# Kernel tuning notes

Measured on AMD Instinct MI355X. Metric: run time of the kernel, lower is better.

## Reference

```python
import jax, jax.numpy as jnp
import numpy as np

GRID = 7
COORD = 5.0
NO_OBJ = 0.5


def _corners(xywh, r, c):
    # xywh: [...,4] with (x_cell, y_cell, w, h); r,c broadcastable grid indices
    x, y, w, h = xywh[..., 0], xywh[..., 1], xywh[..., 2], xywh[..., 3]
    cx = (x + c) / GRID
    cy = (y + r) / GRID
    return cx - w / 2, cy - h / 2, cx + w / 2, cy + h / 2


def _iou(a, b):
    ax1, ay1, ax2, ay2 = a
    bx1, by1, bx2, by2 = b
    iw = jnp.maximum(jnp.minimum(ax2, bx2) - jnp.maximum(ax1, bx1), 0.0)
    ih = jnp.maximum(jnp.minimum(ay2, by2) - jnp.maximum(ay1, by1), 0.0)
    inter = iw * ih
    area_a = (ax2 - ax1) * (ay2 - ay1)
    area_b = (bx2 - bx1) * (by2 - by1)
    union = area_a + area_b - inter
    return jnp.where(union > 0, inter / jnp.where(union > 0, union, 1.0), 0.0)


def setup_inputs() -> dict:
    key = jax.random.key(0)
    k1, k2, k3 = jax.random.split(key, 3)
    B = 8192
    data = jax.random.uniform(k1, (B, GRID, GRID, 30), dtype=jnp.float32)
    labels = jax.random.uniform(k2, (B, GRID, GRID, 30), dtype=jnp.float32)
    # obj flag at channel 4 must be exactly 1 for obj cells
    obj = jax.random.randint(k3, (B, GRID, GRID), 0, 2).astype(jnp.float32)
    labels = labels.at[..., 4].set(obj)
    return {"data": data, "labels": labels}


def reference(data, labels):
    B = data.shape[0]
    r = jnp.arange(GRID, dtype=data.dtype)[None, :, None]  # row index -> y offset
    c = jnp.arange(GRID, dtype=data.dtype)[None, None, :]  # col index -> x offset

    box1 = _corners(data[..., 0:4], r, c)
    box2 = _corners(data[..., 5:9], r, c)
    gt = _corners(labels[..., 0:4], r, c)

    iou1 = _iou(box1, gt)  # [B,7,7]
    iou2 = _iou(box2, gt)
    resp1 = iou1 >= iou2

    xy1 = jnp.sum((data[..., 0:2] - labels[..., 0:2]) ** 2, -1)
    xy2 = jnp.sum((data[..., 5:7] - labels[..., 5:7]) ** 2, -1)
    wh1 = jnp.sum((jnp.sqrt(data[..., 2:4]) - jnp.sqrt(labels[..., 2:4])) ** 2, -1)
    wh2 = jnp.sum((jnp.sqrt(data[..., 7:9]) - jnp.sqrt(labels[..., 7:9])) ** 2, -1)

    d4, d9 = data[..., 4], data[..., 9]
    co = COORD * jnp.where(resp1, xy1, xy2)
    wh = COORD * jnp.where(resp1, wh1, wh2)
    confi = jnp.where(resp1, (d4 - iou1) ** 2, (d9 - iou2) ** 2)
    noobj_in = NO_OBJ * jnp.where(resp1, d9 ** 2, d4 ** 2)
    cls = jnp.sum((data[..., 10:] - labels[..., 10:]) ** 2, -1)

    m = (labels[..., 4] == 1).astype(data.dtype)
    obj_loss = m * (co + wh + confi + noobj_in + cls)
    noobj_loss = (1.0 - m) * NO_OBJ * (d4 ** 2 + d9 ** 2)
    return jnp.sum(obj_loss + noobj_loss) / B
```

## Files before the change

kernel.cpp:

```cpp
#include <hip/hip_runtime.h>

#define COORD 5.0f
#define NO_OBJ 0.5f
#define NCELLS (8192 * 49)
#define INV_B (1.0f / 8192.0f)

#define CPB 128
#define FPT (CPB * 30)
#define NTILES (NCELLS / CPB)
#define NPBLK 512

__device__ __forceinline__ float iou_calc(float ax1, float ay1, float ax2, float ay2,
                                          float bx1, float by1, float bx2, float by2) {
    float iw = fminf(ax2, bx2) - fmaxf(ax1, bx1);
    iw = fmaxf(iw, 0.0f);
    float ih = fminf(ay2, by2) - fmaxf(ay1, by1);
    ih = fmaxf(ih, 0.0f);
    float inter = iw * ih;
    float area_a = (ax2 - ax1) * (ay2 - ay1);
    float area_b = (bx2 - bx1) * (by2 - by1);
    float uni = area_a + area_b - inter;
    return uni > 0.0f ? inter / uni : 0.0f;
}

__device__ __forceinline__ void stage_tile(const float* __restrict__ g, float* s, int tid) {
#pragma unroll
    for (int j = 0; j < 7; j++) {
        __builtin_amdgcn_global_load_lds(
            (const __attribute__((address_space(1))) void*)(g + j * 512 + tid * 4),
            (__attribute__((address_space(3))) void*)(s + j * 512 + tid * 4), 16, 0, 0);
    }
#pragma unroll
    for (int j = 0; j < 2; j++) {
        __builtin_amdgcn_global_load_lds(
            (const __attribute__((address_space(1))) void*)(g + 3584 + j * 128 + tid),
            (__attribute__((address_space(3))) void*)(s + 3584 + j * 128 + tid), 4, 0, 0);
    }
}

__device__ __forceinline__ float cell_loss(const float* __restrict__ sd,
                                           const float* __restrict__ sl,
                                           int idx, int tid) {
    const int cell = idx % 49;
    const float r = (float)(cell / 7);
    const float c = (float)(cell % 7);

    float d[30], l[30];
    const float2* dp = (const float2*)(sd + tid * 30);
    const float2* lp = (const float2*)(sl + tid * 30);
#pragma unroll
    for (int i = 0; i < 15; i++) {
        float2 v = dp[i];
        d[2 * i] = v.x; d[2 * i + 1] = v.y;
        float2 w2 = lp[i];
        l[2 * i] = w2.x; l[2 * i + 1] = w2.y;
    }

    const float inv_g = 1.0f / 7.0f;
    float cx1 = (d[0] + c) * inv_g, cy1 = (d[1] + r) * inv_g;
    float b1x1 = cx1 - d[2] * 0.5f, b1y1 = cy1 - d[3] * 0.5f;
    float b1x2 = cx1 + d[2] * 0.5f, b1y2 = cy1 + d[3] * 0.5f;
    float cx2 = (d[5] + c) * inv_g, cy2 = (d[6] + r) * inv_g;
    float b2x1 = cx2 - d[7] * 0.5f, b2y1 = cy2 - d[8] * 0.5f;
    float b2x2 = cx2 + d[7] * 0.5f, b2y2 = cy2 + d[8] * 0.5f;
    float gx = (l[0] + c) * inv_g, gy = (l[1] + r) * inv_g;
    float gx1 = gx - l[2] * 0.5f, gy1 = gy - l[3] * 0.5f;
    float gx2 = gx + l[2] * 0.5f, gy2 = gy + l[3] * 0.5f;

    float iou1 = iou_calc(b1x1, b1y1, b1x2, b1y2, gx1, gy1, gx2, gy2);
    float iou2 = iou_calc(b2x1, b2y1, b2x2, b2y2, gx1, gy1, gx2, gy2);
    bool resp1 = iou1 >= iou2;

    float xy1 = (d[0] - l[0]) * (d[0] - l[0]) + (d[1] - l[1]) * (d[1] - l[1]);
    float xy2 = (d[5] - l[5]) * (d[5] - l[5]) + (d[6] - l[6]) * (d[6] - l[6]);
    float s2 = sqrtf(d[2]) - sqrtf(l[2]);
    float s3 = sqrtf(d[3]) - sqrtf(l[3]);
    float wh1 = s2 * s2 + s3 * s3;
    float s7 = sqrtf(d[7]) - sqrtf(l[7]);
    float s8 = sqrtf(d[8]) - sqrtf(l[8]);
    float wh2 = s7 * s7 + s8 * s8;

    float d4 = d[4], d9 = d[9];
    float co = COORD * (resp1 ? xy1 : xy2);
    float wh = COORD * (resp1 ? wh1 : wh2);
    float ci = resp1 ? (d4 - iou1) * (d4 - iou1) : (d9 - iou2) * (d9 - iou2);
    float noobj_in = NO_OBJ * (resp1 ? d9 * d9 : d4 * d4);
    float cls = 0.0f;
#pragma unroll
    for (int i = 10; i < 30; i++) {
        float t = d[i] - l[i];
        cls += t * t;
    }

    return (l[4] == 1.0f) ? (co + wh + ci + noobj_in + cls)
                          : NO_OBJ * (d4 * d4 + d9 * d9);
}

__global__ __launch_bounds__(CPB) void yolo_loss_kernel(
    const float* __restrict__ data, const float* __restrict__ labels,
    float* __restrict__ ws) {
    __shared__ float sd[2][FPT];
    __shared__ float sl[2][FPT];

    const int tid = threadIdx.x;
    float acc = 0.0f;
    int cur = 0;

    stage_tile(data + (size_t)blockIdx.x * FPT, sd[0], tid);
    stage_tile(labels + (size_t)blockIdx.x * FPT, sl[0], tid);

    for (int i = blockIdx.x; i < NTILES; i += NPBLK) {
        __syncthreads();
        const int nxt = i + NPBLK;
        if (nxt < NTILES) {
            stage_tile(data + (size_t)nxt * FPT, sd[cur ^ 1], tid);
            stage_tile(labels + (size_t)nxt * FPT, sl[cur ^ 1], tid);
        }
        acc += cell_loss(sd[cur], sl[cur], i * CPB + tid, tid);
        cur ^= 1;
    }
    acc *= INV_B;

#pragma unroll
    for (int off = 32; off > 0; off >>= 1)
        acc += __shfl_down(acc, off, 64);

    __syncthreads();
    if ((tid & 63) == 0) sd[0][tid >> 6] = acc;
    __syncthreads();
    if (tid == 0) ws[blockIdx.x] = sd[0][0] + sd[0][1];
}

__global__ __launch_bounds__(256) void reduce_kernel(const float* __restrict__ ws,
                                                     float* __restrict__ out) {
    float s = 0.0f;
    for (int i = threadIdx.x; i < NPBLK; i += 256) s += ws[i];
#pragma unroll
    for (int off = 32; off > 0; off >>= 1)
        s += __shfl_down(s, off, 64);
    __shared__ float w[4];
    if ((threadIdx.x & 63) == 0) w[threadIdx.x >> 6] = s;
    __syncthreads();
    if (threadIdx.x == 0) out[0] = w[0] + w[1] + w[2] + w[3];
}

extern "C" void kernel_launch(void* const* d_in, const int* in_sizes, int n_in,
                              void* d_out, int out_size, void* d_ws, size_t ws_size,
                              hipStream_t stream) {
    const float* data = (const float*)d_in[0];
    const float* labels = (const float*)d_in[1];
    float* out = (float*)d_out;
    float* ws = (float*)d_ws;

    yolo_loss_kernel<<<NPBLK, CPB, 0, stream>>>(data, labels, ws);
    reduce_kernel<<<1, 256, 0, stream>>>(ws, out);
}
```

Before: 114.4 us.

## Use single-wave blocks with barrier-free two-ahead async prefetch via vmcnt waits

```diff
diff --git a/kernel.cpp b/kernel.cpp
--- a/kernel.cpp
+++ b/kernel.cpp
@@ -5,10 +5,10 @@
 #define NCELLS (8192 * 49)
 #define INV_B (1.0f / 8192.0f)
 
-#define CPB 128
+#define CPB 64
 #define FPT (CPB * 30)
 #define NTILES (NCELLS / CPB)
-#define NPBLK 512
+#define NPBLK 1280
 
 __device__ __forceinline__ float iou_calc(float ax1, float ay1, float ax2, float ay2,
                                           float bx1, float by1, float bx2, float by2) {
@@ -27,14 +27,14 @@
 #pragma unroll
     for (int j = 0; j < 7; j++) {
         __builtin_amdgcn_global_load_lds(
-            (const __attribute__((address_space(1))) void*)(g + j * 512 + tid * 4),
-            (__attribute__((address_space(3))) void*)(s + j * 512 + tid * 4), 16, 0, 0);
+            (const __attribute__((address_space(1))) void*)(g + j * 256 + tid * 4),
+            (__attribute__((address_space(3))) void*)(s + j * 256 + tid * 4), 16, 0, 0);
     }
 #pragma unroll
     for (int j = 0; j < 2; j++) {
         __builtin_amdgcn_global_load_lds(
-            (const __attribute__((address_space(1))) void*)(g + 3584 + j * 128 + tid),
-            (__attribute__((address_space(3))) void*)(s + 3584 + j * 128 + tid), 4, 0, 0);
+            (const __attribute__((address_space(1))) void*)(g + 1792 + j * 64 + tid),
+            (__attribute__((address_space(3))) void*)(s + 1792 + j * 64 + tid), 4, 0, 0);
     }
 }
 
@@ -103,32 +103,39 @@
     __shared__ float sl[2][FPT];
 
     const int tid = threadIdx.x;
+    const int bid = blockIdx.x;
+    const int n = (NTILES - bid + NPBLK - 1) / NPBLK;
+
+    stage_tile(data + (size_t)bid * FPT, sd[0], tid);
+    stage_tile(labels + (size_t)bid * FPT, sl[0], tid);
+    if (n > 1) {
+        const size_t t1 = (size_t)(bid + NPBLK) * FPT;
+        stage_tile(data + t1, sd[1], tid);
+        stage_tile(labels + t1, sl[1], tid);
+    }
+
     float acc = 0.0f;
-    int cur = 0;
-
-    stage_tile(data + (size_t)blockIdx.x * FPT, sd[0], tid);
-    stage_tile(labels + (size_t)blockIdx.x * FPT, sl[0], tid);
-
-    for (int i = blockIdx.x; i < NTILES; i += NPBLK) {
-        __syncthreads();
-        const int nxt = i + NPBLK;
-        if (nxt < NTILES) {
-            stage_tile(data + (size_t)nxt * FPT, sd[cur ^ 1], tid);
-            stage_tile(labels + (size_t)nxt * FPT, sl[cur ^ 1], tid);
+    for (int i = 0; i < n; ++i) {
+        const int cur = i & 1;
+        if (i + 1 < n) {
+            asm volatile("s_waitcnt vmcnt(18)" ::: "memory");
+        } else {
+            asm volatile("s_waitcnt vmcnt(0)" ::: "memory");
         }
-        acc += cell_loss(sd[cur], sl[cur], i * CPB + tid, tid);
-        cur ^= 1;
+        acc += cell_loss(sd[cur], sl[cur], (bid + i * NPBLK) * CPB + tid, tid);
+        if (i + 2 < n) {
+            asm volatile("s_waitcnt lgkmcnt(0)" ::: "memory");
+            const size_t t2 = (size_t)(bid + (i + 2) * NPBLK) * FPT;
+            stage_tile(data + t2, sd[cur], tid);
+            stage_tile(labels + t2, sl[cur], tid);
+        }
     }
     acc *= INV_B;
 
 #pragma unroll
     for (int off = 32; off > 0; off >>= 1)
         acc += __shfl_down(acc, off, 64);
-
-    __syncthreads();
-    if ((tid & 63) == 0) sd[0][tid >> 6] = acc;
-    __syncthreads();
-    if (tid == 0) ws[blockIdx.x] = sd[0][0] + sd[0][1];
+    if (tid == 0) ws[bid] = acc;
 }
 
 __global__ __launch_bounds__(256) void reduce_kernel(const float* __restrict__ ws,
```

Measured after the change: 111.2 us. 2.8% less time.
